# Optimization experiments

Measured on AMD Instinct MI355X. Metric: run time of the kernel, lower is better.

## Reference

```python
import jax, jax.numpy as jnp
import numpy as np

EMBED_DIM = 584  # module-global, used as softmax scale base (C ** -0.5)


def setup_inputs() -> dict:
    key = jax.random.key(0)
    ks = jax.random.split(key, 7)
    B, T, C, H, D = 16, 1024, 584, 8, 73
    x = jax.random.normal(ks[0], (B, T, C), dtype=jnp.float32)
    memory = jax.random.normal(ks[1], (B, T, C), dtype=jnp.float32)
    s = 0.02
    Wq = jax.random.normal(ks[2], (H, C, D), dtype=jnp.float32) * s
    Wk = jax.random.normal(ks[3], (H, C, D), dtype=jnp.float32) * s
    Wv = jax.random.normal(ks[4], (H, C, D), dtype=jnp.float32) * s
    Wp = jax.random.normal(ks[5], (C, C), dtype=jnp.float32) * s
    bp = jnp.zeros((C,), dtype=jnp.float32)
    return {"x": x, "memory": memory, "Wq": Wq, "Wk": Wk, "Wv": Wv, "Wp": Wp, "bp": bp}


def reference(x, memory, Wq, Wk, Wv, Wp, bp):
    B, T, C = x.shape
    # per-head projections, vectorized over heads: [B, H, T, D]
    q = jnp.einsum('btc,hcd->bhtd', x, Wq)
    k = jnp.einsum('bsc,hcd->bhsd', memory, Wk)
    v = jnp.einsum('btc,hcd->bhtd', x, Wv)  # NOTE: value from x, per original code
    # scale uses full embed dim C (not head size), per original code
    scores = jnp.einsum('bhtd,bhsd->bhts', q, k) * (C ** -0.5)
    weights = jax.nn.softmax(scores, axis=-1)
    # dropout is identity in eval/reference mode
    out = jnp.einsum('bhts,bhsd->bhtd', weights, v)  # requires S == T (matches original)
    out = out.transpose(0, 2, 1, 3).reshape(B, T, C)  # concat heads on last dim
    out = out @ Wp + bp  # output projection (dropout identity)
    return out
```

## Files before the change

kernel.cpp:

```cpp
#include <hip/hip_runtime.h>
#include <hip/hip_bf16.h>

typedef unsigned short u16;
typedef __attribute__((ext_vector_type(4))) unsigned short u16x4;
typedef __attribute__((ext_vector_type(8))) unsigned short u16x8;
typedef __attribute__((ext_vector_type(8))) __bf16 bf16x8;
typedef __attribute__((ext_vector_type(4))) float f32x4;

#define BB 16
#define TSEQ 1024
#define CC 584
#define HH 8
#define DHD 73
#define NR (BB*TSEQ)
#define KPW 608
#define KIT 19
#define DP 96
#define HD (HH*DP)
#define NP3 640
#define LP 40
#define PPITCH 88
#define CEXP 0.0596985934f

__device__ __forceinline__ u16 f2bf(float f) {
  __bf16 h = (__bf16)f;
  return __builtin_bit_cast(u16, h);
}
__device__ __forceinline__ bf16x8 as_bf(u16x8 v) { return __builtin_bit_cast(bf16x8, v); }

#define PKA 9728
#define PKB 5472
#define PKC 1520
__global__ void pack_all_kernel(const float* __restrict__ x, const float* __restrict__ mem,
                                const float* __restrict__ Wq, const float* __restrict__ Wk,
                                const float* __restrict__ Wv, const float* __restrict__ Wp,
                                u16* __restrict__ xmb, u16* __restrict__ wt,
                                u16* __restrict__ wpt) {
  const int bidx = blockIdx.x;
  const int tid = threadIdx.x;
  if (bidx < PKA) {
    int idx = bidx * 256 + tid;
    int row = idx / (KPW / 8);
    int c8  = (idx % (KPW / 8)) * 8;
    u16x8 o = {0, 0, 0, 0, 0, 0, 0, 0};
    if (c8 < CC) {
      const float* src = (row < NR) ? &x[(size_t)row * CC + c8]
                                    : &mem[(size_t)(row - NR) * CC + c8];
      f32x4 a = *(const f32x4*)src;
      f32x4 b = *(const f32x4*)(src + 4);
#pragma unroll
      for (int t = 0; t < 4; t++) { o[t] = f2bf(a[t]); o[4 + t] = f2bf(b[t]); }
    }
    *(u16x8*)&xmb[(size_t)row * KPW + c8] = o;
  } else if (bidx < PKA + PKB) {
    int idx = (bidx - PKA) * 256 + tid;
    int w   = idx / (HD * KPW);
    int rem = idx % (HD * KPW);
    int n = rem / KPW;
    int k = rem % KPW;
    int h = n / DP, d = n % DP;
    u16 val = 0;
    if (d < DHD && k < CC) {
      const float* W = (w == 0) ? Wq : ((w == 1) ? Wv : Wk);
      val = f2bf(W[((size_t)h * CC + k) * DHD + d]);
    }
    wt[idx] = val;
  } else {
    int idx = (bidx - PKA - PKB) * 256 + tid;
    int n = idx / KPW;
    int c = idx % KPW;
    u16 val = 0;
    if (n < CC && c < CC) val = f2bf(Wp[(size_t)c * CC + n]);
    wpt[idx] = val;
  }
}

template <int MODE>
__global__ __launch_bounds__(256) void gemm_bt_kernel(
    const u16* __restrict__ A, const u16* __restrict__ Bt,
    void* __restrict__ CoutV, void* __restrict__ CoutV2,
    const float* __restrict__ bias) {
  const int mx = blockIdx.x;
  const bool isMem = (MODE == 4) && (mx >= 128);
  if (MODE == 4 && isMem && blockIdx.y >= 6) return;
  const int m0 = mx * 128;
  const int n0 = (MODE == 4) ? ((isMem ? 1536 : 0) + blockIdx.y * 128)
                             : blockIdx.y * 128;

  __shared__ u16 As[128 * LP];
  __shared__ u16 Bs[128 * LP];
  const int tid  = threadIdx.x;
  const int lane = tid & 63;
  const int wave = tid >> 6;
  const int wm = (wave >> 1) * 64;
  const int wn = (wave & 1) * 64;
  const int q15  = lane & 15;
  const int quad = lane >> 4;

  f32x4 acc[4][4];
#pragma unroll
  for (int i = 0; i < 4; i++)
#pragma unroll
    for (int j = 0; j < 4; j++) acc[i][j] = (f32x4){0.f, 0.f, 0.f, 0.f};

  const int r0 = tid >> 2;
  const int c0 = (tid & 3) * 8;
  const u16* gA0 = &A[(size_t)(m0 + r0) * KPW + c0];
  const u16* gA1 = gA0 + (size_t)64 * KPW;
  const u16* gB0 = &Bt[(size_t)(n0 + r0) * KPW + c0];
  const u16* gB1 = gB0 + (size_t)64 * KPW;

  u16x8 ra0 = *(const u16x8*)gA0;
  u16x8 ra1 = *(const u16x8*)gA1;
  u16x8 rb0 = *(const u16x8*)gB0;
  u16x8 rb1 = *(const u16x8*)gB1;

  for (int kk = 0; kk < KIT; ++kk) {
    *(u16x8*)&As[r0 * LP + c0]        = ra0;
    *(u16x8*)&As[(r0 + 64) * LP + c0] = ra1;
    *(u16x8*)&Bs[r0 * LP + c0]        = rb0;
    *(u16x8*)&Bs[(r0 + 64) * LP + c0] = rb1;
    __syncthreads();

    if (kk < KIT - 1) {
      const int kb = (kk + 1) * 32;
      ra0 = *(const u16x8*)&gA0[kb];
      ra1 = *(const u16x8*)&gA1[kb];
      rb0 = *(const u16x8*)&gB0[kb];
      rb1 = *(const u16x8*)&gB1[kb];
    }

    bf16x8 af[4], bfr[4];
#pragma unroll
    for (int i = 0; i < 4; i++)
      af[i] = as_bf(*(const u16x8*)&As[(wm + i * 16 + q15) * LP + quad * 8]);
#pragma unroll
    for (int j = 0; j < 4; j++)
      bfr[j] = as_bf(*(const u16x8*)&Bs[(wn + j * 16 + q15) * LP + quad * 8]);
#pragma unroll
    for (int i = 0; i < 4; i++)
#pragma unroll
      for (int j = 0; j < 4; j++)
        acc[i][j] = __builtin_amdgcn_mfma_f32_16x16x32_bf16(af[i], bfr[j], acc[i][j], 0, 0, 0);
    __syncthreads();
  }

#pragma unroll
  for (int i = 0; i < 4; i++) {
#pragma unroll
    for (int j = 0; j < 4; j++) {
      const int row = m0 + wm + i * 16 + quad * 4;
      const int col = n0 + wn + j * 16 + q15;
      if (MODE == 4) {
        if (isMem) {
          u16* Cout = (u16*)CoutV2;
          const int rk = row - NR;
          const int ck = col - 1536;
#pragma unroll
          for (int r = 0; r < 4; r++)
            Cout[(size_t)(rk + r) * HD + ck] = f2bf(acc[i][j][r]);
        } else if (col < HD) {
          u16* Cout = (u16*)CoutV;
#pragma unroll
          for (int r = 0; r < 4; r++)
            Cout[(size_t)(row + r) * HD + col] = f2bf(acc[i][j][r]);
        } else {
          u16* Cout = (u16*)CoutV;
          const int vn = col - HD;
          const int b  = row >> 10;
          const int tl = row & 1023;
          u16x4 pk;
#pragma unroll
          for (int r = 0; r < 4; r++) pk[r] = f2bf(acc[i][j][r]);
          *(u16x4*)&Cout[(size_t)(NR * HD) + ((size_t)(b * HD + vn)) * TSEQ + tl] = pk;
        }
      } else {
        if (col < CC) {
          float* Cout = (float*)CoutV;
          const float bv = bias[col];
#pragma unroll
          for (int r = 0; r < 4; r++)
            Cout[(size_t)(row + r) * CC + col] = acc[i][j][r] + bv;
        }
      }
    }
  }
}

__global__ __launch_bounds__(256, 3) void attn_kernel(
    const u16* __restrict__ qb, const u16* __restrict__ kb,
    const u16* __restrict__ vt, u16* __restrict__ attn) {
  __shared__ u16 smem[128 * 96 + 64 * 104 + 96 * 72];
  u16* Qs = smem;
  u16* Ks = smem + 128 * 96;
  u16* Vs = smem + 128 * 96 + 64 * 104;
  u16* Pt = smem;

  const int tid  = threadIdx.x;
  const int lane = tid & 63;
  const int wave = tid >> 6;
  const int q15  = lane & 15;
  const int quad = lane >> 4;
  const int bid  = blockIdx.x;
  const int loc  = bid >> 3;
  const int pair = (bid & 7) * 16 + (loc >> 3);
  const int b  = pair >> 3;
  const int h  = pair & 7;
  const int t0 = (loc & 7) * 128;
  const int wq0 = wave * 32;

  int krow[3], kc[3], vrow[3], vc[3];
#pragma unroll
  for (int p = 0; p < 3; p++) {
    int qk = tid + 256 * p;
    krow[p] = qk / 12; kc[p] = (qk % 12) * 8;
    int qv = tid + 256 * p;
    vrow[p] = qv / 8;  vc[p] = (qv % 8) * 8;
  }
  const u16* kbase = &kb[(size_t)(b * TSEQ) * HD + h * DP];
  const u16* vbase = &vt[(size_t)(b * HD + h * DP) * TSEQ];

  for (int q = tid; q < 128 * 12; q += 256) {
    int row = q / 12, c8 = (q % 12) * 8;
    *(u16x8*)&Qs[row * 96 + c8] =
        *(const u16x8*)&qb[(size_t)(b * TSEQ + t0 + row) * HD + h * DP + c8];
  }
  if (tid < 128) {
    const u16x8 z = {0, 0, 0, 0, 0, 0, 0, 0};
    size_t base = (size_t)(b * TSEQ + t0 + tid) * KPW + CC;
    *(u16x8*)&attn[base] = z;
    *(u16x8*)&attn[base + 8] = z;
    *(u16x8*)&attn[base + 16] = z;
  }
  __syncthreads();

  bf16x8 aq[2][3];
#pragma unroll
  for (int n = 0; n < 2; n++)
#pragma unroll
    for (int kcx = 0; kcx < 3; kcx++)
      aq[n][kcx] = as_bf(*(const u16x8*)&Qs[(wq0 + n * 16 + q15) * 96 + kcx * 32 + quad * 8]);

  float lsum[2] = {0.f, 0.f};
  f32x4 oacc[2][6];
#pragma unroll
  for (int m = 0; m < 2; m++)
#pragma unroll
    for (int jd = 0; jd < 6; jd++) oacc[m][jd] = (f32x4){0.f, 0.f, 0.f, 0.f};

  u16* Ptw = &Pt[wave * 32 * PPITCH];

  u16x8 kreg[3], vreg[3];
#pragma unroll
  for (int p = 0; p < 3; p++) {
    kreg[p] = *(const u16x8*)&kbase[(size_t)krow[p] * HD + kc[p]];
    vreg[p] = *(const u16x8*)&vbase[(size_t)vrow[p] * TSEQ + vc[p]];
  }

  for (int si = 0; si < 16; ++si) {
#pragma unroll
    for (int p = 0; p < 3; p++) {
      *(u16x8*)&Ks[krow[p] * 104 + kc[p]] = kreg[p];
      *(u16x8*)&Vs[vrow[p] * 72 + vc[p]]  = vreg[p];
    }
    __syncthreads();

    if (si < 15) {
      const int s1 = (si + 1) * 64;
#pragma unroll
      for (int p = 0; p < 3; p++) {
        kreg[p] = *(const u16x8*)&kbase[(size_t)(s1 + krow[p]) * HD + kc[p]];
        vreg[p] = *(const u16x8*)&vbase[(size_t)vrow[p] * TSEQ + s1 + vc[p]];
      }
    }

    f32x4 st[4][2];
#pragma unroll
    for (int mt = 0; mt < 4; mt++)
#pragma unroll
      for (int n = 0; n < 2; n++) st[mt][n] = (f32x4){0.f, 0.f, 0.f, 0.f};
#pragma unroll
    for (int kcx = 0; kcx < 3; kcx++) {
      bf16x8 ak[4];
#pragma unroll
      for (int mt = 0; mt < 4; mt++)
        ak[mt] = as_bf(*(const u16x8*)&Ks[(mt * 16 + q15) * 104 + kcx * 32 + quad * 8]);
#pragma unroll
      for (int mt = 0; mt < 4; mt++)
#pragma unroll
        for (int n = 0; n < 2; n++)
          st[mt][n] = __builtin_amdgcn_mfma_f32_16x16x32_bf16(ak[mt], aq[n][kcx], st[mt][n], 0, 0, 0);
    }

#pragma unroll
    for (int mt = 0; mt < 4; mt++)
#pragma unroll
      for (int n = 0; n < 2; n++) {
        f32x4 pv;
#pragma unroll
        for (int r = 0; r < 4; r++) pv[r] = __builtin_amdgcn_exp2f(st[mt][n][r] * CEXP);
        lsum[n] += (pv[0] + pv[1]) + (pv[2] + pv[3]);
        u16x4 pk;
#pragma unroll
        for (int r = 0; r < 4; r++) pk[r] = f2bf(pv[r]);
        *(u16x4*)&Ptw[(n * 16 + q15) * PPITCH + mt * 16 + quad * 4] = pk;
      }

#pragma unroll
    for (int kcx = 0; kcx < 2; kcx++) {
      bf16x8 ap[2];
#pragma unroll
      for (int m = 0; m < 2; m++)
        ap[m] = as_bf(*(const u16x8*)&Ptw[(m * 16 + q15) * PPITCH + kcx * 32 + quad * 8]);
#pragma unroll
      for (int jd = 0; jd < 6; jd++) {
        bf16x8 bv = as_bf(*(const u16x8*)&Vs[(jd * 16 + q15) * 72 + kcx * 32 + quad * 8]);
#pragma unroll
        for (int m = 0; m < 2; m++)
          oacc[m][jd] = __builtin_amdgcn_mfma_f32_16x16x32_bf16(ap[m], bv, oacc[m][jd], 0, 0, 0);
      }
    }
    __syncthreads();
  }

  float lr[2];
#pragma unroll
  for (int n = 0; n < 2; n++) {
    float s = lsum[n];
    s += __shfl_xor(s, 16);
    s += __shfl_xor(s, 32);
    lr[n] = s;
  }

#pragma unroll
  for (int m = 0; m < 2; m++) {
#pragma unroll
    for (int r = 0; r < 4; r++) {
      const float inv = 1.f / __shfl(lr[m], quad * 4 + r);
      const int trow = t0 + wq0 + m * 16 + quad * 4 + r;
#pragma unroll
      for (int jd = 0; jd < 5; jd++) {
        const int d = jd * 16 + q15;
        if (d < DHD)
          attn[(size_t)(b * TSEQ + trow) * KPW + h * DHD + d] = f2bf(oacc[m][jd][r] * inv);
      }
    }
  }
}


extern "C" void kernel_launch(void* const* d_in, const int* in_sizes, int n_in,
                              void* d_out, int out_size, void* d_ws, size_t ws_size,
                              hipStream_t stream) {
  const float* x   = (const float*)d_in[0];
  const float* mem = (const float*)d_in[1];
  const float* Wq  = (const float*)d_in[2];
  const float* Wk  = (const float*)d_in[3];
  const float* Wv  = (const float*)d_in[4];
  const float* Wp  = (const float*)d_in[5];
  const float* bp  = (const float*)d_in[6];
  float* out = (float*)d_out;

  char* ws = (char*)d_ws;
  const size_t SZ_XMB = (size_t)2 * NR * KPW * 2;
  const size_t SZ_WT  = (size_t)3 * HD * KPW * 2;
  const size_t SZ_WPT = (size_t)NP3 * KPW * 2;
  const size_t SZ_QB  = (size_t)NR * HD * 2;

  u16* xmb    = (u16*)(ws);
  u16* attn_o = (u16*)(ws);
  u16* wt     = (u16*)(ws + SZ_XMB);
  u16* wp_t   = (u16*)(ws + SZ_XMB + SZ_WT);
  u16* q_buf  = (u16*)(ws + SZ_XMB + SZ_WT + SZ_WPT);
  u16* vt_buf = q_buf + (size_t)NR * HD;
  u16* k_buf  = (u16*)(ws + SZ_XMB + SZ_WT + SZ_WPT + 2 * SZ_QB);

  (void)in_sizes; (void)n_in; (void)out_size; (void)ws_size;

  pack_all_kernel<<<PKA + PKB + PKC, 256, 0, stream>>>(x, mem, Wq, Wk, Wv, Wp,
                                                       xmb, wt, wp_t);

  dim3 gproj(256, 12);
  gemm_bt_kernel<4><<<gproj, 256, 0, stream>>>(xmb, wt, q_buf, k_buf, nullptr);

  attn_kernel<<<BB * HH * (TSEQ / 128), 256, 0, stream>>>(q_buf, k_buf, vt_buf, attn_o);

  dim3 g3(NR / 128, NP3 / 128);
  gemm_bt_kernel<2><<<g3, 256, 0, stream>>>(attn_o, wp_t, out, nullptr, bp);
}
```

Measured before the change: 298.0 us.

## Fuse fp32-to-bf16 activation conversion into projection GEMM A-tile loads

The projection GEMM now reads x and memory directly as fp32 and converts to bf16 while staging tiles into shared memory. This removes the separate packing pass and the padded bf16 activation buffer, and the K tail past column 584 is zero-filled in registers instead. The 2D grid with early-exit blocks becomes a flat 1D grid, and the LDS row pitch drops from 40 to 32 elements. The trade-off is that each fp32 A tile is reread by every column block, roughly doubling A-side load bytes, plus conversion work inside the GEMM loop. The unpadded pitch may also cause LDS bank conflicts on fragment reads.

```diff
diff --git a/kernel.cpp b/kernel.cpp
--- a/kernel.cpp
+++ b/kernel.cpp
@@ -18,7 +18,6 @@
 #define DP 96
 #define HD (HH*DP)
 #define NP3 640
-#define LP 40
 #define PPITCH 88
 #define CEXP 0.0596985934f
 
@@ -28,32 +27,15 @@
 }
 __device__ __forceinline__ bf16x8 as_bf(u16x8 v) { return __builtin_bit_cast(bf16x8, v); }
 
-#define PKA 9728
 #define PKB 5472
 #define PKC 1520
-__global__ void pack_all_kernel(const float* __restrict__ x, const float* __restrict__ mem,
-                                const float* __restrict__ Wq, const float* __restrict__ Wk,
-                                const float* __restrict__ Wv, const float* __restrict__ Wp,
-                                u16* __restrict__ xmb, u16* __restrict__ wt,
-                                u16* __restrict__ wpt) {
+__global__ void pack_w_kernel(const float* __restrict__ Wq, const float* __restrict__ Wk,
+                              const float* __restrict__ Wv, const float* __restrict__ Wp,
+                              u16* __restrict__ wt, u16* __restrict__ wpt) {
   const int bidx = blockIdx.x;
   const int tid = threadIdx.x;
-  if (bidx < PKA) {
+  if (bidx < PKB) {
     int idx = bidx * 256 + tid;
-    int row = idx / (KPW / 8);
-    int c8  = (idx % (KPW / 8)) * 8;
-    u16x8 o = {0, 0, 0, 0, 0, 0, 0, 0};
-    if (c8 < CC) {
-      const float* src = (row < NR) ? &x[(size_t)row * CC + c8]
-                                    : &mem[(size_t)(row - NR) * CC + c8];
-      f32x4 a = *(const f32x4*)src;
-      f32x4 b = *(const f32x4*)(src + 4);
-#pragma unroll
-      for (int t = 0; t < 4; t++) { o[t] = f2bf(a[t]); o[4 + t] = f2bf(b[t]); }
-    }
-    *(u16x8*)&xmb[(size_t)row * KPW + c8] = o;
-  } else if (bidx < PKA + PKB) {
-    int idx = (bidx - PKA) * 256 + tid;
     int w   = idx / (HD * KPW);
     int rem = idx % (HD * KPW);
     int n = rem / KPW;
@@ -66,7 +48,7 @@
     }
     wt[idx] = val;
   } else {
-    int idx = (bidx - PKA - PKB) * 256 + tid;
+    int idx = (bidx - PKB) * 256 + tid;
     int n = idx / KPW;
     int c = idx % KPW;
     u16 val = 0;
@@ -77,18 +59,26 @@
 
 template <int MODE>
 __global__ __launch_bounds__(256) void gemm_bt_kernel(
-    const u16* __restrict__ A, const u16* __restrict__ Bt,
-    void* __restrict__ CoutV, void* __restrict__ CoutV2,
+    const void* __restrict__ Av, const void* __restrict__ Amv,
+    const u16* __restrict__ Bt,
+    void* __restrict__ C1, void* __restrict__ C2,
     const float* __restrict__ bias) {
-  const int mx = blockIdx.x;
-  const bool isMem = (MODE == 4) && (mx >= 128);
-  if (MODE == 4 && isMem && blockIdx.y >= 6) return;
+  int mx, ny;
+  bool isMem = false;
+  if (MODE == 4) {
+    const int bid = blockIdx.x;
+    isMem = bid >= 1536;
+    const int rr = isMem ? bid - 1536 : bid;
+    mx = rr & 127;
+    ny = rr >> 7;
+  } else {
+    mx = blockIdx.x; ny = blockIdx.y;
+  }
   const int m0 = mx * 128;
-  const int n0 = (MODE == 4) ? ((isMem ? 1536 : 0) + blockIdx.y * 128)
-                             : blockIdx.y * 128;
-
-  __shared__ u16 As[128 * LP];
-  __shared__ u16 Bs[128 * LP];
+  const int n0 = (MODE == 4 && isMem) ? (1536 + ny * 128) : (ny * 128);
+
+  __shared__ u16 As[128 * 32];
+  __shared__ u16 Bs[128 * 32];
   const int tid  = threadIdx.x;
   const int lane = tid & 63;
   const int wave = tid >> 6;
@@ -105,38 +95,69 @@
 
   const int r0 = tid >> 2;
   const int c0 = (tid & 3) * 8;
-  const u16* gA0 = &A[(size_t)(m0 + r0) * KPW + c0];
-  const u16* gA1 = gA0 + (size_t)64 * KPW;
+
   const u16* gB0 = &Bt[(size_t)(n0 + r0) * KPW + c0];
   const u16* gB1 = gB0 + (size_t)64 * KPW;
-
-  u16x8 ra0 = *(const u16x8*)gA0;
-  u16x8 ra1 = *(const u16x8*)gA1;
   u16x8 rb0 = *(const u16x8*)gB0;
   u16x8 rb1 = *(const u16x8*)gB1;
 
+  const float* pA0f = nullptr; const float* pA1f = nullptr;
+  const u16*   pA0h = nullptr; const u16*   pA1h = nullptr;
+  f32x4 ral0, rah0, ral1, rah1;
+  u16x8 ha0, ha1;
+  const f32x4 fz = (f32x4){0.f, 0.f, 0.f, 0.f};
+  if (MODE == 4) {
+    const float* gA = isMem ? (const float*)Amv : (const float*)Av;
+    pA0f = &gA[(size_t)(m0 + r0) * CC + c0];
+    pA1f = pA0f + (size_t)64 * CC;
+    ral0 = *(const f32x4*)pA0f; rah0 = *(const f32x4*)(pA0f + 4);
+    ral1 = *(const f32x4*)pA1f; rah1 = *(const f32x4*)(pA1f + 4);
+  } else {
+    pA0h = &((const u16*)Av)[(size_t)(m0 + r0) * KPW + c0];
+    pA1h = pA0h + (size_t)64 * KPW;
+    ha0 = *(const u16x8*)pA0h;
+    ha1 = *(const u16x8*)pA1h;
+  }
+
   for (int kk = 0; kk < KIT; ++kk) {
-    *(u16x8*)&As[r0 * LP + c0]        = ra0;
-    *(u16x8*)&As[(r0 + 64) * LP + c0] = ra1;
-    *(u16x8*)&Bs[r0 * LP + c0]        = rb0;
-    *(u16x8*)&Bs[(r0 + 64) * LP + c0] = rb1;
+    u16x8 wa0, wa1;
+    if (MODE == 4) {
+#pragma unroll
+      for (int t = 0; t < 4; t++) {
+        wa0[t] = f2bf(ral0[t]); wa0[4 + t] = f2bf(rah0[t]);
+        wa1[t] = f2bf(ral1[t]); wa1[4 + t] = f2bf(rah1[t]);
+      }
+    } else { wa0 = ha0; wa1 = ha1; }
+    *(u16x8*)&As[r0 * 32 + c0]        = wa0;
+    *(u16x8*)&As[(r0 + 64) * 32 + c0] = wa1;
+    *(u16x8*)&Bs[r0 * 32 + c0]        = rb0;
+    *(u16x8*)&Bs[(r0 + 64) * 32 + c0] = rb1;
     __syncthreads();
 
     if (kk < KIT - 1) {
       const int kb = (kk + 1) * 32;
-      ra0 = *(const u16x8*)&gA0[kb];
-      ra1 = *(const u16x8*)&gA1[kb];
       rb0 = *(const u16x8*)&gB0[kb];
       rb1 = *(const u16x8*)&gB1[kb];
+      if (MODE == 4) {
+        if (kk < 17 || c0 == 0) {
+          ral0 = *(const f32x4*)&pA0f[kb]; rah0 = *(const f32x4*)&pA0f[kb + 4];
+          ral1 = *(const f32x4*)&pA1f[kb]; rah1 = *(const f32x4*)&pA1f[kb + 4];
+        } else {
+          ral0 = fz; rah0 = fz; ral1 = fz; rah1 = fz;
+        }
+      } else {
+        ha0 = *(const u16x8*)&pA0h[kb];
+        ha1 = *(const u16x8*)&pA1h[kb];
+      }
     }
 
     bf16x8 af[4], bfr[4];
 #pragma unroll
     for (int i = 0; i < 4; i++)
-      af[i] = as_bf(*(const u16x8*)&As[(wm + i * 16 + q15) * LP + quad * 8]);
+      af[i] = as_bf(*(const u16x8*)&As[(wm + i * 16 + q15) * 32 + quad * 8]);
 #pragma unroll
     for (int j = 0; j < 4; j++)
-      bfr[j] = as_bf(*(const u16x8*)&Bs[(wn + j * 16 + q15) * LP + quad * 8]);
+      bfr[j] = as_bf(*(const u16x8*)&Bs[(wn + j * 16 + q15) * 32 + quad * 8]);
 #pragma unroll
     for (int i = 0; i < 4; i++)
 #pragma unroll
@@ -153,19 +174,18 @@
       const int col = n0 + wn + j * 16 + q15;
       if (MODE == 4) {
         if (isMem) {
-          u16* Cout = (u16*)CoutV2;
-          const int rk = row - NR;
+          u16* Cout = (u16*)C2;
           const int ck = col - 1536;
 #pragma unroll
           for (int r = 0; r < 4; r++)
-            Cout[(size_t)(rk + r) * HD + ck] = f2bf(acc[i][j][r]);
+            Cout[(size_t)(row + r) * HD + ck] = f2bf(acc[i][j][r]);
         } else if (col < HD) {
-          u16* Cout = (u16*)CoutV;
+          u16* Cout = (u16*)C1;
 #pragma unroll
           for (int r = 0; r < 4; r++)
             Cout[(size_t)(row + r) * HD + col] = f2bf(acc[i][j][r]);
         } else {
-          u16* Cout = (u16*)CoutV;
+          u16* Cout = (u16*)C1;
           const int vn = col - HD;
           const int b  = row >> 10;
           const int tl = row & 1023;
@@ -176,7 +196,7 @@
         }
       } else {
         if (col < CC) {
-          float* Cout = (float*)CoutV;
+          float* Cout = (float*)C1;
           const float bv = bias[col];
 #pragma unroll
           for (int r = 0; r < 4; r++)
@@ -362,29 +382,26 @@
   float* out = (float*)d_out;
 
   char* ws = (char*)d_ws;
-  const size_t SZ_XMB = (size_t)2 * NR * KPW * 2;
+  const size_t SZ_AO  = (size_t)NR * KPW * 2;
   const size_t SZ_WT  = (size_t)3 * HD * KPW * 2;
   const size_t SZ_WPT = (size_t)NP3 * KPW * 2;
   const size_t SZ_QB  = (size_t)NR * HD * 2;
 
-  u16* xmb    = (u16*)(ws);
   u16* attn_o = (u16*)(ws);
-  u16* wt     = (u16*)(ws + SZ_XMB);
-  u16* wp_t   = (u16*)(ws + SZ_XMB + SZ_WT);
-  u16* q_buf  = (u16*)(ws + SZ_XMB + SZ_WT + SZ_WPT);
+  u16* wt     = (u16*)(ws + SZ_AO);
+  u16* wp_t   = (u16*)(ws + SZ_AO + SZ_WT);
+  u16* q_buf  = (u16*)(ws + SZ_AO + SZ_WT + SZ_WPT);
   u16* vt_buf = q_buf + (size_t)NR * HD;
-  u16* k_buf  = (u16*)(ws + SZ_XMB + SZ_WT + SZ_WPT + 2 * SZ_QB);
+  u16* k_buf  = (u16*)(ws + SZ_AO + SZ_WT + SZ_WPT + 2 * SZ_QB);
 
   (void)in_sizes; (void)n_in; (void)out_size; (void)ws_size;
 
-  pack_all_kernel<<<PKA + PKB + PKC, 256, 0, stream>>>(x, mem, Wq, Wk, Wv, Wp,
-                                                       xmb, wt, wp_t);
-
-  dim3 gproj(256, 12);
-  gemm_bt_kernel<4><<<gproj, 256, 0, stream>>>(xmb, wt, q_buf, k_buf, nullptr);
+  pack_w_kernel<<<PKB + PKC, 256, 0, stream>>>(Wq, Wk, Wv, Wp, wt, wp_t);
+
+  gemm_bt_kernel<4><<<2304, 256, 0, stream>>>(x, mem, wt, q_buf, k_buf, nullptr);
 
   attn_kernel<<<BB * HH * (TSEQ / 128), 256, 0, stream>>>(q_buf, k_buf, vt_buf, attn_o);
 
-  dim3 g3(NR / 128, NP3 / 128);
-  gemm_bt_kernel<2><<<g3, 256, 0, stream>>>(attn_o, wp_t, out, nullptr, bp);
+  dim3 g3(128, 5);
+  gemm_bt_kernel<2><<<g3, 256, 0, stream>>>(attn_o, nullptr, wp_t, out, nullptr, bp);
 }
```

Result: slower. 313.2 us (+5.1%).
